# Kernel optimization log

Hardware: AMD Instinct MI355X
Metric: run time of the kernel (lower is better)

## Reference

```python
import jax, jax.numpy as jnp
import numpy as np

# sparse_shape = output_shape[1:4] + [1, 0, 0]
D, H, W = 41, 160, 160
EPS = 1e-3          # BatchNorm1d eps from functools.partial
NEG = -1e30         # -inf surrogate for masked max-pool


def _conv(x, w):
    # submanifold 3x3x3 conv, bias=False; x: [B,D,H,W,C], w: [3,3,3,Ci,Co]
    return jax.lax.conv_general_dilated(
        x, w, (1, 1, 1), 'SAME', dimension_numbers=('NDHWC', 'DHWIO', 'NDHWC'))


def _bn_relu(x, mask, g, b, m, v):
    # BatchNorm1d (eval semantics, running stats) + ReLU, restricted to active voxels
    y = (x - m) * jax.lax.rsqrt(v + EPS) * g + b
    return jnp.where(mask, jnp.maximum(y, 0.0), 0.0)


def _pool(x, mask, kernel, stride, pad):
    # SparseMaxPool3d: max over ACTIVE inputs in window; output active iff any input active
    k = (1,) + kernel + (1,)
    s = (1,) + stride + (1,)
    p = ((0, 0),) + tuple((q, q) for q in pad) + ((0, 0),)
    y = jax.lax.reduce_window(jnp.where(mask, x, NEG), NEG, jax.lax.max, k, s, p)
    m = jax.lax.reduce_window(mask, False, jnp.logical_or, k, s, p)
    return jnp.where(m, y, 0.0), m


def setup_inputs():
    key = jax.random.key(0)
    ks = jax.random.split(key, 16)
    N, Cin = 80000, 16
    vf = jax.random.normal(ks[0], (N, Cin), jnp.float32)
    b = jnp.zeros((N, 1), jnp.int32)
    z = jax.random.randint(ks[1], (N, 1), 0, D)
    yy = jax.random.randint(ks[2], (N, 1), 0, H)
    xx = jax.random.randint(ks[3], (N, 1), 0, W)
    coors = jnp.concatenate([b, z, yy, xx], axis=1)  # [N, 4] = (batch, z, y, x)
    w_in = jax.random.normal(ks[4], (3, 3, 3, Cin, 32), jnp.float32) * 0.05
    w_up = jax.random.normal(ks[5], (3, 3, 3, 32, 64), jnp.float32) * 0.05
    w_mid = jax.random.normal(ks[6], (6, 3, 3, 3, 64, 64), jnp.float32) * 0.05
    bn0_gamma = jax.random.uniform(ks[7], (32,), jnp.float32, 0.5, 1.5)
    bn0_beta = jax.random.normal(ks[8], (32,), jnp.float32) * 0.1
    bn0_mean = jax.random.normal(ks[9], (32,), jnp.float32) * 0.1
    bn0_var = jax.random.uniform(ks[10], (32,), jnp.float32, 0.5, 1.5)
    bn_gamma = jax.random.uniform(ks[11], (10, 64), jnp.float32, 0.5, 1.5)
    bn_beta = jax.random.normal(ks[12], (10, 64), jnp.float32) * 0.1
    bn_mean = jax.random.normal(ks[13], (10, 64), jnp.float32) * 0.1
    bn_var = jax.random.uniform(ks[14], (10, 64), jnp.float32, 0.5, 1.5)
    return dict(voxel_features=vf, coors=coors, batch_size=1,
                w_in=w_in, w_up=w_up, w_mid=w_mid,
                bn0_gamma=bn0_gamma, bn0_beta=bn0_beta, bn0_mean=bn0_mean, bn0_var=bn0_var,
                bn_gamma=bn_gamma, bn_beta=bn_beta, bn_mean=bn_mean, bn_var=bn_var)


def reference(voxel_features, coors, batch_size, w_in, w_up, w_mid,
              bn0_gamma, bn0_beta, bn0_mean, bn0_var,
              bn_gamma, bn_beta, bn_mean, bn_var):
    B = int(batch_size)
    Cin = voxel_features.shape[-1]
    idx = (coors[:, 0], coors[:, 1], coors[:, 2], coors[:, 3])
    # SparseConvTensor -> dense grid + active-site mask (submanifold conv only
    # produces outputs at active sites, so dense conv + mask is the same math)
    x = jnp.zeros((B, D, H, W, Cin), voxel_features.dtype).at[idx].set(voxel_features)
    mask = jnp.zeros((B, D, H, W), bool).at[idx].set(True)[..., None]
    # block 0 (indice_key subm0)
    x = _bn_relu(_conv(x, w_in), mask, bn0_gamma, bn0_beta, bn0_mean, bn0_var)
    x = _bn_relu(_conv(x, w_up), mask, bn_gamma[0], bn_beta[0], bn_mean[0], bn_var[0])
    x, mask = _pool(x, mask, (3, 3, 3), (2, 1, 1), (1, 1, 1))  # D: 41 -> 21
    x = _bn_relu(x, mask, bn_gamma[1], bn_beta[1], bn_mean[1], bn_var[1])
    # block 1 (indice_key subm1)
    for i in range(3):
        x = _bn_relu(_conv(x, w_mid[i]), mask,
                     bn_gamma[2 + i], bn_beta[2 + i], bn_mean[2 + i], bn_var[2 + i])
    x, mask = _pool(x, mask, (3, 3, 3), (2, 1, 1), (0, 1, 1))  # D: 21 -> 10
    x = _bn_relu(x, mask, bn_gamma[5], bn_beta[5], bn_mean[5], bn_var[5])
    # block 2 (indice_key subm2)
    for i in range(3):
        x = _bn_relu(_conv(x, w_mid[3 + i]), mask,
                     bn_gamma[6 + i], bn_beta[6 + i], bn_mean[6 + i], bn_var[6 + i])
    x, mask = _pool(x, mask, (3, 1, 1), (2, 1, 1), (0, 0, 0))  # D: 10 -> 4
    x = _bn_relu(x, mask, bn_gamma[9], bn_beta[9], bn_mean[9], bn_var[9])
    # .dense() -> [B,C,D',H,W] then view(B, C*D', H, W)
    x = jnp.transpose(x, (0, 4, 1, 2, 3))
    b, c, d, h, w = x.shape
    return x.reshape(b, c * d, h, w)
```

## Files before the change

kernel.cpp:

```cpp
#include <hip/hip_runtime.h>
#include <hip/hip_bf16.h>
#include <stdint.h>


#define EPS 1e-3f
constexpr int Dd = 41, Hh = 160, Ww = 160;
constexpr int D1 = 21, D2 = 10;

typedef short bf16x8 __attribute__((ext_vector_type(8)));
typedef short short8 __attribute__((ext_vector_type(8)));
typedef float f32x4  __attribute__((ext_vector_type(4)));

static __device__ __forceinline__ short f2bfs(float f) {
    __hip_bfloat16 h = __float2bfloat16(f);
    return *reinterpret_cast<short*>(&h);
}
static __device__ __forceinline__ float bfs2f(short s) {
    union { unsigned u; float f; } cv;
    cv.u = ((unsigned)(unsigned short)s) << 16;
    return cv.f;
}
static __device__ __forceinline__ short8 smax8(short8 a, short8 b) {
    short8 r;
    #pragma unroll
    for (int j = 0; j < 8; ++j) r[j] = a[j] > b[j] ? a[j] : b[j];
    return r;
}

__global__ void k_scatter_winner(const int* __restrict__ coors, int* __restrict__ map, int N) {
    int i = blockIdx.x * blockDim.x + threadIdx.x;
    if (i >= N) return;
    int z = coors[i*4+1], y = coors[i*4+2], x = coors[i*4+3];
    atomicMax(&map[(z*Hh + y)*Ww + x], i);
}

__global__ void k_conv1(const float* __restrict__ feat, const int* __restrict__ coors,
                        const int* __restrict__ map, const float* __restrict__ w,
                        const float* __restrict__ g, const float* __restrict__ b,
                        const float* __restrict__ mn, const float* __restrict__ vr,
                        float* __restrict__ y1, int N) {
    int t = blockIdx.x * blockDim.x + threadIdx.x;
    int i = t >> 5, oc = t & 31;
    if (i >= N) return;
    int z = coors[i*4+1], yy = coors[i*4+2], xx = coors[i*4+3];
    int cell = (z*Hh + yy)*Ww + xx;
    if (map[cell] != i) return;
    float acc = 0.f;
    for (int dz = 0; dz < 3; ++dz) {
        int nz = z + dz - 1; if (nz < 0 || nz >= Dd) continue;
        for (int dy = 0; dy < 3; ++dy) {
            int ny = yy + dy - 1; if (ny < 0 || ny >= Hh) continue;
            for (int dx = 0; dx < 3; ++dx) {
                int nx = xx + dx - 1; if (nx < 0 || nx >= Ww) continue;
                int j = map[(nz*Hh + ny)*Ww + nx];
                if (j < 0) continue;
                const float* f = feat + j*16;
                const float* wp = w + ((dz*3+dy)*3+dx)*(16*32) + oc;
                #pragma unroll
                for (int ic = 0; ic < 16; ++ic)
                    acc += f[ic] * wp[ic*32];
            }
        }
    }
    float s = g[oc] * rsqrtf(vr[oc] + EPS);
    y1[i*32 + oc] = fmaxf((acc - mn[oc]) * s + b[oc], 0.f);
}

__global__ void k_conv2(const float* __restrict__ y1, const int* __restrict__ coors,
                        const int* __restrict__ map, const float* __restrict__ w,
                        const float* __restrict__ g, const float* __restrict__ b,
                        const float* __restrict__ mn, const float* __restrict__ vr,
                        float* __restrict__ y2, int N) {
    int t = blockIdx.x * blockDim.x + threadIdx.x;
    int i = t >> 6, oc = t & 63;
    if (i >= N) return;
    int z = coors[i*4+1], yy = coors[i*4+2], xx = coors[i*4+3];
    int cell = (z*Hh + yy)*Ww + xx;
    if (map[cell] != i) return;
    float acc = 0.f;
    for (int dz = 0; dz < 3; ++dz) {
        int nz = z + dz - 1; if (nz < 0 || nz >= Dd) continue;
        for (int dy = 0; dy < 3; ++dy) {
            int ny = yy + dy - 1; if (ny < 0 || ny >= Hh) continue;
            for (int dx = 0; dx < 3; ++dx) {
                int nx = xx + dx - 1; if (nx < 0 || nx >= Ww) continue;
                int j = map[(nz*Hh + ny)*Ww + nx];
                if (j < 0) continue;
                const float* f = y1 + j*32;
                const float* wp = w + ((dz*3+dy)*3+dx)*(32*64) + oc;
                #pragma unroll
                for (int ic = 0; ic < 32; ++ic)
                    acc += f[ic] * wp[ic*64];
            }
        }
    }
    float s = g[oc] * rsqrtf(vr[oc] + EPS);
    y2[i*64 + oc] = fmaxf((acc - mn[oc]) * s + b[oc], 0.f);
}

__global__ void k_p1zg(const float* __restrict__ y2, const int* __restrict__ map,
                       short8* __restrict__ out) {
    int t = blockIdx.x * blockDim.x + threadIdx.x;
    if (t >= D1*Hh*Ww*8) return;
    int c8 = t & 7, vox = t >> 3;
    int x = vox % Ww, y = (vox / Ww) % Hh, zo = vox / (Ww*Hh);
    float mv[8];
    #pragma unroll
    for (int q = 0; q < 8; ++q) mv[q] = 0.f;
    bool any = false;
    for (int dz = 0; dz < 3; ++dz) {
        int zi = 2*zo + dz - 1;
        if ((unsigned)zi >= (unsigned)Dd) continue;
        int j = map[(zi*Hh + y)*Ww + x];
        if (j < 0) continue;
        any = true;
        const float4* f = reinterpret_cast<const float4*>(y2 + (size_t)j*64 + c8*8);
        float4 a = f[0], b = f[1];
        mv[0] = fmaxf(mv[0], a.x); mv[1] = fmaxf(mv[1], a.y);
        mv[2] = fmaxf(mv[2], a.z); mv[3] = fmaxf(mv[3], a.w);
        mv[4] = fmaxf(mv[4], b.x); mv[5] = fmaxf(mv[5], b.y);
        mv[6] = fmaxf(mv[6], b.z); mv[7] = fmaxf(mv[7], b.w);
    }
    short8 o;
    #pragma unroll
    for (int q = 0; q < 8; ++q) o[q] = any ? f2bfs(mv[q]) : (short)0xFF80;
    out[(size_t)vox*8 + c8] = o;
}

__global__ void k_p1y(const short8* __restrict__ in, short8* __restrict__ out) {
    int t = blockIdx.x * blockDim.x + threadIdx.x;
    if (t >= D1*Hh*Ww*8) return;
    int c8 = t & 7, vox = t >> 3;
    int x = vox % Ww, y = (vox / Ww) % Hh, zo = vox / (Ww*Hh);
    size_t base = ((size_t)zo*Hh*Ww)*8;
    short8 m = in[base + ((size_t)y*Ww + x)*8 + c8];
    if (y > 0)      m = smax8(m, in[base + ((size_t)(y-1)*Ww + x)*8 + c8]);
    if (y < Hh-1)   m = smax8(m, in[base + ((size_t)(y+1)*Ww + x)*8 + c8]);
    out[(size_t)vox*8 + c8] = m;
}

__global__ void k_p1x(const short8* __restrict__ in,
                      const float* __restrict__ g, const float* __restrict__ b,
                      const float* __restrict__ mn, const float* __restrict__ vr,
                      short8* __restrict__ out, uint8_t* __restrict__ mk) {
    int t = blockIdx.x * blockDim.x + threadIdx.x;
    if (t >= D1*Hh*Ww*8) return;
    int c8 = t & 7, vox = t >> 3;
    int x = vox % Ww;
    short8 m = in[(size_t)vox*8 + c8];
    if (x > 0)      m = smax8(m, in[(size_t)(vox-1)*8 + c8]);
    if (x < Ww-1)   m = smax8(m, in[(size_t)(vox+1)*8 + c8]);
    bool occ = m[0] >= 0;
    short8 o;
    #pragma unroll
    for (int j = 0; j < 8; ++j) {
        float v = 0.f;
        if (occ) {
            int c = c8*8 + j;
            float s = g[c] * rsqrtf(vr[c] + EPS);
            v = fmaxf(bfs2f(m[j])*s + (b[c] - mn[c]*s), 0.f);
        }
        o[j] = f2bfs(v);
    }
    out[(size_t)vox*8 + c8] = o;
    if (c8 == 0) mk[vox] = occ ? 1 : 0;
}

__global__ void k_pack_w(const float* __restrict__ w, __hip_bfloat16* __restrict__ wp, int total) {
    int idx = blockIdx.x * blockDim.x + threadIdx.x;
    if (idx >= total) return;
    int j    = idx & 7;
    int lane = (idx >> 3) & 63;
    int n    = (idx >> 9) & 3;
    int h    = (idx >> 11) & 1;
    int rest = idx >> 12;
    int t    = rest % 27;
    int L    = rest / 27;
    int ic = h*32 + (lane >> 4)*8 + j;
    int oc = n*16 + (lane & 15);
    wp[idx] = __float2bfloat16(w[((size_t)(L*27 + t)*64 + ic)*64 + oc]);
}

template<int DD>
__global__ __launch_bounds__(256, 3) void k_conv64_mfma(
        const __hip_bfloat16* __restrict__ in, const __hip_bfloat16* __restrict__ wpL,
        const uint8_t* __restrict__ mask,
        const float* __restrict__ g, const float* __restrict__ b,
        const float* __restrict__ mn, const float* __restrict__ vr,
        __hip_bfloat16* __restrict__ out) {
    __shared__ short8 sA[10*34*8];
    const int tid = threadIdx.x;
    const int w = tid >> 6, l = tid & 63;
    const int l15 = l & 15, kg = l >> 4;
    const int x0 = blockIdx.x * 32, y0 = blockIdx.y * 8, z = blockIdx.z;
    const int yb = y0 + 2*w;

    f32x4 acc[4][4];
    #pragma unroll
    for (int f = 0; f < 4; ++f)
        #pragma unroll
        for (int n = 0; n < 4; ++n)
            acc[f][n] = (f32x4){0.f, 0.f, 0.f, 0.f};

    for (int kz = 0; kz < 3; ++kz) {
        const int zi = z + kz - 1;
        if (zi < 0 || zi >= DD) continue;
        __syncthreads();
        for (int c = tid; c < 2720; c += 256) {
            int v = c >> 3, s = c & 7;
            int ly = v / 34, lx = v - ly*34;
            int gy = y0 - 1 + ly, gx = x0 - 1 + lx;
            bf16x8 val = {0,0,0,0,0,0,0,0};
            if ((unsigned)gy < (unsigned)Hh && (unsigned)gx < (unsigned)Ww)
                val = *reinterpret_cast<const bf16x8*>(
                        in + ((size_t)(zi*Hh + gy)*Ww + gx)*64 + s*8);
            sA[v*8 + (s ^ (lx & 7))] = val;
        }
        __syncthreads();
        #pragma unroll
        for (int ky = 0; ky < 3; ++ky) {
            #pragma unroll
            for (int kx = 0; kx < 3; ++kx) {
                const int t = (kz*3 + ky)*3 + kx;
                #pragma unroll
                for (int h = 0; h < 2; ++h) {
                    bf16x8 bfr[4];
                    const __hip_bfloat16* wb = wpL + (size_t)(t*2 + h)*2048 + (size_t)l*8;
                    #pragma unroll
                    for (int n = 0; n < 4; ++n)
                        bfr[n] = *reinterpret_cast<const bf16x8*>(wb + n*512);
                    bf16x8 afr[4];
                    #pragma unroll
                    for (int f = 0; f < 4; ++f) {
                        int ly = 2*w + (f >> 1) + ky;
                        int lx = (f & 1)*16 + l15 + kx;
                        afr[f] = sA[(ly*34 + lx)*8 + ((h*4 + kg) ^ (lx & 7))];
                    }
                    #pragma unroll
                    for (int f = 0; f < 4; ++f)
                        #pragma unroll
                        for (int n = 0; n < 4; ++n)
                            acc[f][n] = __builtin_amdgcn_mfma_f32_16x16x32_bf16(
                                afr[f], bfr[n], acc[f][n], 0, 0, 0);
                }
            }
        }
    }

    float sc[4], sh[4];
    #pragma unroll
    for (int n = 0; n < 4; ++n) {
        int oc = n*16 + l15;
        float s = g[oc] * rsqrtf(vr[oc] + EPS);
        sc[n] = s; sh[n] = b[oc] - mn[oc]*s;
    }
    #pragma unroll
    for (int f = 0; f < 4; ++f) {
        int yv = yb + (f >> 1);
        int xb2 = x0 + (f & 1)*16 + kg*4;
        #pragma unroll
        for (int r = 0; r < 4; ++r) {
            int vox = (z*Hh + yv)*Ww + (xb2 + r);
            bool mk = mask[vox] != 0;
            #pragma unroll
            for (int n = 0; n < 4; ++n) {
                float v = mk ? fmaxf(acc[f][n][r]*sc[n] + sh[n], 0.f) : 0.f;
                out[(size_t)vox*64 + n*16 + l15] = __float2bfloat16(v);
            }
        }
    }
}

__global__ void k_p2z(const short8* __restrict__ in, const uint8_t* __restrict__ mki,
                      short8* __restrict__ out, uint8_t* __restrict__ occ) {
    int t = blockIdx.x * blockDim.x + threadIdx.x;
    if (t >= D2*Hh*Ww*8) return;
    int c8 = t & 7, vox = t >> 3;
    int x = vox % Ww, y = (vox / Ww) % Hh, zo = vox / (Ww*Hh);
    short8 m = {0,0,0,0,0,0,0,0};
    uint8_t o = 0;
    for (int dz = 0; dz < 3; ++dz) {
        int zi = 2*zo + dz;
        int cv = (zi*Hh + y)*Ww + x;
        m = smax8(m, in[(size_t)cv*8 + c8]);
        if (c8 == 0) o |= mki[cv];
    }
    out[(size_t)vox*8 + c8] = m;
    if (c8 == 0) occ[vox] = o;
}

__global__ void k_p2y(const short8* __restrict__ in, const uint8_t* __restrict__ occi,
                      short8* __restrict__ out, uint8_t* __restrict__ occ) {
    int t = blockIdx.x * blockDim.x + threadIdx.x;
    if (t >= D2*Hh*Ww*8) return;
    int c8 = t & 7, vox = t >> 3;
    int x = vox % Ww, y = (vox / Ww) % Hh, zo = vox / (Ww*Hh);
    size_t base = (size_t)zo*Hh*Ww;
    short8 m = in[(base + (size_t)y*Ww + x)*8 + c8];
    uint8_t o = (c8 == 0) ? occi[base + (size_t)y*Ww + x] : 0;
    if (y > 0) {
        m = smax8(m, in[(base + (size_t)(y-1)*Ww + x)*8 + c8]);
        if (c8 == 0) o |= occi[base + (size_t)(y-1)*Ww + x];
    }
    if (y < Hh-1) {
        m = smax8(m, in[(base + (size_t)(y+1)*Ww + x)*8 + c8]);
        if (c8 == 0) o |= occi[base + (size_t)(y+1)*Ww + x];
    }
    out[(size_t)vox*8 + c8] = m;
    if (c8 == 0) occ[vox] = o;
}

__global__ void k_p2x(const short8* __restrict__ in, const uint8_t* __restrict__ occi,
                      const float* __restrict__ g, const float* __restrict__ b,
                      const float* __restrict__ mn, const float* __restrict__ vr,
                      short8* __restrict__ out, uint8_t* __restrict__ mk) {
    int t = blockIdx.x * blockDim.x + threadIdx.x;
    if (t >= D2*Hh*Ww*8) return;
    int c8 = t & 7, vox = t >> 3;
    int x = vox % Ww;
    short8 m = in[(size_t)vox*8 + c8];
    uint8_t occ = occi[vox];
    if (x > 0)    { m = smax8(m, in[(size_t)(vox-1)*8 + c8]); occ |= occi[vox-1]; }
    if (x < Ww-1) { m = smax8(m, in[(size_t)(vox+1)*8 + c8]); occ |= occi[vox+1]; }
    short8 o;
    #pragma unroll
    for (int j = 0; j < 8; ++j) {
        float v = 0.f;
        if (occ) {
            int c = c8*8 + j;
            float s = g[c] * rsqrtf(vr[c] + EPS);
            v = fmaxf(bfs2f(m[j])*s + (b[c] - mn[c]*s), 0.f);
        }
        o[j] = f2bfs(v);
    }
    out[(size_t)vox*8 + c8] = o;
    if (c8 == 0) mk[vox] = occ ? 1 : 0;
}

__global__ __launch_bounds__(256) void k_pool3t(
        const short8* __restrict__ in, const uint8_t* __restrict__ mki,
        const float* __restrict__ g, const float* __restrict__ b,
        const float* __restrict__ mn, const float* __restrict__ vr,
        float* __restrict__ out) {
    __shared__ float lds[32][65];
    const int tid = threadIdx.x;
    const int x0 = blockIdx.x * 32, y = blockIdx.y, zo = blockIdx.z;
    {
        int xq = tid >> 3, c8 = tid & 7;
        int x = x0 + xq;
        short8 m = {0,0,0,0,0,0,0,0};
        bool occ = false;
        for (int dz = 0; dz < 3; ++dz) {
            int zi = 2*zo + dz;
            int cv = (zi*Hh + y)*Ww + x;
            m = smax8(m, in[(size_t)cv*8 + c8]);
            occ = occ || (mki[cv] != 0);
        }
        #pragma unroll
        for (int j = 0; j < 8; ++j) {
            float v = 0.f;
            if (occ) {
                int c = c8*8 + j;
                float s = g[c] * rsqrtf(vr[c] + EPS);
                v = fmaxf(bfs2f(m[j])*s + (b[c] - mn[c]*s), 0.f);
            }
            lds[xq][c8*8 + j] = v;
        }
    }
    __syncthreads();
    {
        int c = tid >> 2, xo = (tid & 3) * 8;
        size_t row = ((size_t)(c*4 + zo)*Hh + y)*Ww + x0 + xo;
        #pragma unroll
        for (int j = 0; j < 8; ++j)
            out[row + j] = lds[xo + j][c];
    }
}

extern "C" void kernel_launch(void* const* d_in, const int* in_sizes, int n_in,
                              void* d_out, int out_size, void* d_ws, size_t ws_size,
                              hipStream_t stream) {
    const float* vf    = (const float*)d_in[0];
    const int*   coors = (const int*)  d_in[1];
    const float* w_in  = (const float*)d_in[3];
    const float* w_up  = (const float*)d_in[4];
    const float* w_mid = (const float*)d_in[5];
    const float* bn0_g = (const float*)d_in[6];
    const float* bn0_b = (const float*)d_in[7];
    const float* bn0_m = (const float*)d_in[8];
    const float* bn0_v = (const float*)d_in[9];
    const float* bn_g  = (const float*)d_in[10];
    const float* bn_b  = (const float*)d_in[11];
    const float* bn_m  = (const float*)d_in[12];
    const float* bn_v  = (const float*)d_in[13];
    const int N = in_sizes[0] / 16;

    char* ws = (char*)d_ws;
    size_t off = 0;
    auto alloc = [&](size_t bytes) {
        void* p = ws + off;
        off = (off + bytes + 255) & ~(size_t)255;
        return p;
    };
    int*            map  = (int*)            alloc((size_t)Dd*Hh*Ww*4);
    float*          y1   = (float*)          alloc((size_t)N*32*4);
    float*          y2   = (float*)          alloc((size_t)N*64*4);
    uint8_t*        mk1  = (uint8_t*)        alloc((size_t)D1*Hh*Ww);
    uint8_t*        mk2  = (uint8_t*)        alloc((size_t)D2*Hh*Ww);
    uint8_t*        occa = (uint8_t*)        alloc((size_t)D2*Hh*Ww);
    uint8_t*        occb = (uint8_t*)        alloc((size_t)D2*Hh*Ww);
    __hip_bfloat16* wp   = (__hip_bfloat16*) alloc((size_t)6*27*2*4*64*8*2);
    short8*         A    = (short8*)         alloc((size_t)D1*Hh*Ww*64*2);
    short8*         B    = (short8*)         alloc((size_t)D1*Hh*Ww*64*2);
    const size_t D2G = (size_t)D2*Hh*Ww*64*2;
    short8* p2a = A;
    short8* p2b = (short8*)((char*)A + D2G);
    short8* Bq  = B;
    short8* Aq  = A;

    const int PACK_TOTAL = 6*27*2*4*64*8;
    const size_t WPL = (size_t)27*2*4*64*8;
    const int P1T = D1*Hh*Ww*8, P2T = D2*Hh*Ww*8;

    hipMemsetAsync(map, 0xFF, (size_t)Dd*Hh*Ww*4, stream);
    k_pack_w<<<(PACK_TOTAL + 255)/256, 256, 0, stream>>>(w_mid, wp, PACK_TOTAL);
    k_scatter_winner<<<(N + 255)/256, 256, 0, stream>>>(coors, map, N);
    k_conv1<<<(N*32 + 255)/256, 256, 0, stream>>>(vf, coors, map, w_in,
            bn0_g, bn0_b, bn0_m, bn0_v, y1, N);
    k_conv2<<<(N*64 + 255)/256, 256, 0, stream>>>(y1, coors, map, w_up,
            bn_g, bn_b, bn_m, bn_v, y2, N);

    k_p1zg<<<(P1T + 255)/256, 256, 0, stream>>>(y2, map, A);
    k_p1y <<<(P1T + 255)/256, 256, 0, stream>>>(A, B);
    k_p1x <<<(P1T + 255)/256, 256, 0, stream>>>(B,
            bn_g + 64, bn_b + 64, bn_m + 64, bn_v + 64, A, mk1);

    dim3 g1(Ww/32, Hh/8, D1);
    k_conv64_mfma<D1><<<g1, 256, 0, stream>>>((const __hip_bfloat16*)A, wp + 0*WPL, mk1,
            bn_g + 2*64, bn_b + 2*64, bn_m + 2*64, bn_v + 2*64, (__hip_bfloat16*)B);
    k_conv64_mfma<D1><<<g1, 256, 0, stream>>>((const __hip_bfloat16*)B, wp + 1*WPL, mk1,
            bn_g + 3*64, bn_b + 3*64, bn_m + 3*64, bn_v + 3*64, (__hip_bfloat16*)A);
    k_conv64_mfma<D1><<<g1, 256, 0, stream>>>((const __hip_bfloat16*)A, wp + 2*WPL, mk1,
            bn_g + 4*64, bn_b + 4*64, bn_m + 4*64, bn_v + 4*64, (__hip_bfloat16*)B);

    k_p2z<<<(P2T + 255)/256, 256, 0, stream>>>(B, mk1, p2a, occa);
    k_p2y<<<(P2T + 255)/256, 256, 0, stream>>>(p2a, occa, p2b, occb);
    k_p2x<<<(P2T + 255)/256, 256, 0, stream>>>(p2b, occb,
            bn_g + 5*64, bn_b + 5*64, bn_m + 5*64, bn_v + 5*64, Bq, mk2);

    dim3 g2(Ww/32, Hh/8, D2);
    k_conv64_mfma<D2><<<g2, 256, 0, stream>>>((const __hip_bfloat16*)Bq, wp + 3*WPL, mk2,
            bn_g + 6*64, bn_b + 6*64, bn_m + 6*64, bn_v + 6*64, (__hip_bfloat16*)Aq);
    k_conv64_mfma<D2><<<g2, 256, 0, stream>>>((const __hip_bfloat16*)Aq, wp + 4*WPL, mk2,
            bn_g + 7*64, bn_b + 7*64, bn_m + 7*64, bn_v + 7*64, (__hip_bfloat16*)Bq);
    k_conv64_mfma<D2><<<g2, 256, 0, stream>>>((const __hip_bfloat16*)Bq, wp + 5*WPL, mk2,
            bn_g + 8*64, bn_b + 8*64, bn_m + 8*64, bn_v + 8*64, (__hip_bfloat16*)Aq);

    dim3 g3(Ww/32, Hh, 4);
    k_pool3t<<<g3, 256, 0, stream>>>(Aq, mk2,
            bn_g + 9*64, bn_b + 9*64, bn_m + 9*64, bn_v + 9*64, (float*)d_out);
}
```

Before: 1.504 ms.

## Prefetch next z-slice into registers while computing current slice in conv64

```diff
diff --git a/kernel.cpp b/kernel.cpp
--- a/kernel.cpp
+++ b/kernel.cpp
@@ -195,6 +195,25 @@
     const int x0 = blockIdx.x * 32, y0 = blockIdx.y * 8, z = blockIdx.z;
     const int yb = y0 + 2*w;
 
+    int ldsoff[11], goff[11];
+    bool gok[11];
+    #pragma unroll
+    for (int i = 0; i < 11; ++i) {
+        int c = tid + i*256;
+        bool cok = (c < 2720);
+        int cc = cok ? c : 0;
+        int v = cc >> 3, s = cc & 7;
+        int ly = v / 34, lx = v - ly*34;
+        int gy = y0 - 1 + ly, gx = x0 - 1 + lx;
+        gok[i] = cok && (unsigned)gy < (unsigned)Hh && (unsigned)gx < (unsigned)Ww;
+        goff[i] = (gy*Ww + gx)*64 + s*8;
+        ldsoff[i] = cok ? (v*8 + (s ^ (lx & 7))) : -1;
+    }
+
+    bool vz[3];
+    #pragma unroll
+    for (int kz = 0; kz < 3; ++kz) { int zi = z + kz - 1; vz[kz] = (zi >= 0) && (zi < DD); }
+
     f32x4 acc[4][4];
     #pragma unroll
     for (int f = 0; f < 4; ++f)
@@ -202,49 +221,63 @@
         for (int n = 0; n < 4; ++n)
             acc[f][n] = (f32x4){0.f, 0.f, 0.f, 0.f};
 
+    const bf16x8 zero8 = {0,0,0,0,0,0,0,0};
+    bf16x8 st[11];
+    {
+        int zb = (z - 1) * (Hh*Ww*64);
+        #pragma unroll
+        for (int i = 0; i < 11; ++i)
+            st[i] = (vz[0] && gok[i])
+                  ? *reinterpret_cast<const bf16x8*>(in + zb + goff[i]) : zero8;
+    }
+
+    #pragma unroll
     for (int kz = 0; kz < 3; ++kz) {
-        const int zi = z + kz - 1;
-        if (zi < 0 || zi >= DD) continue;
+        if (vz[kz]) {
+            #pragma unroll
+            for (int i = 0; i < 11; ++i)
+                if (ldsoff[i] >= 0) sA[ldsoff[i]] = st[i];
+        }
+        if (kz < 2) {
+            int zb = (z + kz) * (Hh*Ww*64);
+            bool vn = vz[kz+1];
+            #pragma unroll
+            for (int i = 0; i < 11; ++i)
+                st[i] = (vn && gok[i])
+                      ? *reinterpret_cast<const bf16x8*>(in + zb + goff[i]) : zero8;
+        }
         __syncthreads();
-        for (int c = tid; c < 2720; c += 256) {
-            int v = c >> 3, s = c & 7;
-            int ly = v / 34, lx = v - ly*34;
-            int gy = y0 - 1 + ly, gx = x0 - 1 + lx;
-            bf16x8 val = {0,0,0,0,0,0,0,0};
-            if ((unsigned)gy < (unsigned)Hh && (unsigned)gx < (unsigned)Ww)
-                val = *reinterpret_cast<const bf16x8*>(
-                        in + ((size_t)(zi*Hh + gy)*Ww + gx)*64 + s*8);
-            sA[v*8 + (s ^ (lx & 7))] = val;
-        }
-        __syncthreads();
-        #pragma unroll
-        for (int ky = 0; ky < 3; ++ky) {
+        if (vz[kz]) {
             #pragma unroll
-            for (int kx = 0; kx < 3; ++kx) {
-                const int t = (kz*3 + ky)*3 + kx;
+            for (int ky = 0; ky < 3; ++ky) {
                 #pragma unroll
-                for (int h = 0; h < 2; ++h) {
-                    bf16x8 bfr[4];
-                    const __hip_bfloat16* wb = wpL + (size_t)(t*2 + h)*2048 + (size_t)l*8;
+                for (int kx = 0; kx < 3; ++kx) {
+                    const int t = (kz*3 + ky)*3 + kx;
                     #pragma unroll
-                    for (int n = 0; n < 4; ++n)
-                        bfr[n] = *reinterpret_cast<const bf16x8*>(wb + n*512);
-                    bf16x8 afr[4];
-                    #pragma unroll
-                    for (int f = 0; f < 4; ++f) {
-                        int ly = 2*w + (f >> 1) + ky;
-                        int lx = (f & 1)*16 + l15 + kx;
-                        afr[f] = sA[(ly*34 + lx)*8 + ((h*4 + kg) ^ (lx & 7))];
-                    }
-                    #pragma unroll
-                    for (int f = 0; f < 4; ++f)
+                    for (int h = 0; h < 2; ++h) {
+                        bf16x8 bfr[4];
+                        const __hip_bfloat16* wb = wpL + (size_t)(t*2 + h)*2048 + (size_t)l*8;
                         #pragma unroll
                         for (int n = 0; n < 4; ++n)
-                            acc[f][n] = __builtin_amdgcn_mfma_f32_16x16x32_bf16(
-                                afr[f], bfr[n], acc[f][n], 0, 0, 0);
+                            bfr[n] = *reinterpret_cast<const bf16x8*>(wb + n*512);
+                        bf16x8 afr[4];
+                        #pragma unroll
+                        for (int f = 0; f < 4; ++f) {
+                            int ly = 2*w + (f >> 1) + ky;
+                            int lx = (f & 1)*16 + l15 + kx;
+                            afr[f] = sA[(ly*34 + lx)*8 + ((h*4 + kg) ^ (lx & 7))];
+                        }
+                        #pragma unroll
+                        for (int f = 0; f < 4; ++f)
+                            #pragma unroll
+                            for (int n = 0; n < 4; ++n)
+                                acc[f][n] = __builtin_amdgcn_mfma_f32_16x16x32_bf16(
+                                    afr[f], bfr[n], acc[f][n], 0, 0, 0);
+                    }
                 }
             }
         }
+        __syncthreads();
     }
 
     float sc[4], sh[4];
```

Result: slower. 1.630 ms (+8.3%).
